# Kernel optimization log

Measured on AMD Instinct MI355X. Metric: run time of the kernel, lower is better.

The kernel has to match this reference:

```python
import jax, jax.numpy as jnp
import numpy as np

B, D, H, M, N, S = 256, 256, 512, 64, 2048, 3
SHIFTS = (1, 0, -1)  # = range(S//2, -S//2, -1); matches np.roll(eye, s, axis=1) one-hot matrices


def setup_inputs():
    key = jax.random.key(0)
    k = jax.random.split(key, 24)
    f32 = jnp.float32

    def rn(i, shape, scale):
        return jax.random.normal(k[i], shape, f32) * scale

    rh = jax.random.uniform(k[3], (B, N), f32)
    wh = jax.random.uniform(k[4], (B, N), f32)
    sc_ih = 1.0 / np.sqrt(D + M)
    sc_h = 1.0 / np.sqrt(H)
    return dict(
        inp=rn(0, (B, D), 1.0),
        h_tm1=rn(1, (B, H), 0.1),
        c_tm1=rn(2, (B, H), 0.1),
        read_head_tm1=rh / rh.sum(1, keepdims=True),
        write_head_tm1=wh / wh.sum(1, keepdims=True),
        memory=rn(5, (B, N, M), 0.5),
        W_ih=rn(6, (4 * H, D + M), sc_ih), W_hh=rn(7, (4 * H, H), sc_h),
        b_ih=jnp.zeros((4 * H,), f32), b_hh=jnp.zeros((4 * H,), f32),
        W_rk=rn(8, (M, H), sc_h), b_rk=rn(9, (M,), 0.01),
        W_wk=rn(10, (M, H), sc_h), b_wk=rn(11, (M,), 0.01),
        W_rc=rn(12, (3, H), sc_h), b_rc=jnp.zeros((3,), f32),
        W_wc=rn(13, (3, H), sc_h), b_wc=jnp.zeros((3,), f32),
        W_rs=rn(14, (S, H), sc_h), b_rs=jnp.zeros((S,), f32),
        W_ws=rn(15, (S, H), sc_h), b_ws=jnp.zeros((S,), f32),
        W_w=rn(16, (2 * M, H), sc_h), b_w=jnp.zeros((2 * M,), f32),
    )


def _head_params(h, Wk, bk, Wc, bc, Ws, bs):
    kk = jnp.tanh(h @ Wk.T + bk)                     # [B,M] key
    c = h @ Wc.T + bc                                # [B,3]
    beta = jax.nn.relu(c[:, 0:1]) + 1e-4             # focus strength
    g = jax.nn.sigmoid(c[:, 1:2])                    # interpolation gate
    gamma = jax.nn.relu(c[:, 2:3]) + 1.0001          # sharpening power
    s = jax.nn.softmax(h @ Ws.T + bs, axis=1)        # [B,S] shift weights
    return kk, s, beta, g, gamma


def _address(memory, head_tm1, kk, s, beta, g, gamma):
    dot = jnp.einsum('bm,bnm->bn', kk, memory)
    nk = jnp.linalg.norm(kk, axis=1, keepdims=True)  # [B,1]
    nM = jnp.linalg.norm(memory, axis=2)             # [B,N]
    cos = dot / jnp.maximum(nk * nM, 1e-8)
    content = jax.nn.softmax(beta * cos, axis=1)
    inter = g * content + (1.0 - g) * head_tm1       # gated interpolation [B,N]
    # circular shift; identical math to contracting with the one-hot C tensor
    rolled = jnp.stack([jnp.roll(inter, -sh, axis=1) for sh in SHIFTS], axis=1)  # [B,S,N]
    out = jnp.einsum('bsn,bs->bn', rolled, s)
    out = out ** gamma                               # sharpen
    return out / out.sum(1, keepdims=True)


def reference(inp, h_tm1, c_tm1, read_head_tm1, write_head_tm1, memory,
              W_ih, W_hh, b_ih, b_hh, W_rk, b_rk, W_wk, b_wk,
              W_rc, b_rc, W_wc, b_wc, W_rs, b_rs, W_ws, b_ws, W_w, b_w):
    # read addressing uses previous hidden state
    rp = _head_params(h_tm1, W_rk, b_rk, W_rc, b_rc, W_rs, b_rs)
    read_head = _address(memory, read_head_tm1, *rp)
    M_read = jnp.einsum('bn,bnm->bm', read_head, memory)  # [B,M]
    # LSTMCell controller (torch gate order i,f,g,o)
    x = jnp.concatenate([inp, M_read], axis=1)
    z = x @ W_ih.T + b_ih + h_tm1 @ W_hh.T + b_hh
    zi, zf, zg, zo = jnp.split(z, 4, axis=1)
    c_t = jax.nn.sigmoid(zf) * c_tm1 + jax.nn.sigmoid(zi) * jnp.tanh(zg)
    h_t = jax.nn.sigmoid(zo) * jnp.tanh(c_t)
    # write addressing uses new hidden state
    wp = _head_params(h_t, W_wk, b_wk, W_wc, b_wc, W_ws, b_ws)
    write_head = _address(memory, write_head_tm1, *wp)
    wa = h_t @ W_w.T + b_w
    e = jax.nn.sigmoid(wa[:, :M])                    # erase
    a = jnp.tanh(wa[:, M:])                          # add
    ww = write_head[:, :, None]                      # [B,N,1]
    M_out = memory * (1.0 - ww * e[:, None, :]) + ww * a[:, None, :]
    return (h_t, c_t, read_head, write_head, M_out)
```

## Files before the change

### kernel.cpp

```cpp
#include <hip/hip_runtime.h>
#include <hip/hip_bf16.h>

#define Bb 256
#define Dd 256
#define Hh 512
#define Mm 64
#define Nn 2048

typedef __attribute__((ext_vector_type(8))) short bf16x8;
typedef __attribute__((ext_vector_type(4))) float f32x4;

static __device__ __forceinline__ short f2bf(float f) {
    unsigned u = __float_as_uint(f);
    unsigned r = (u + 0x7FFFu + ((u >> 16) & 1u)) >> 16;
    return (short)r;
}

__global__ __launch_bounds__(256) void head_params_kernel(
    const float* __restrict__ h,
    const float* __restrict__ Wk, const float* __restrict__ bk,
    const float* __restrict__ Wc, const float* __restrict__ bc,
    const float* __restrict__ Ws, const float* __restrict__ bs,
    float* __restrict__ kk, float* __restrict__ par)
{
    int b = blockIdx.x;
    __shared__ float hs[Hh];
    __shared__ float red[6];
    __shared__ float skk[Mm];
    const float* hb = h + (size_t)b * Hh;
    for (int i = threadIdx.x; i < Hh; i += 256) hs[i] = hb[i];
    __syncthreads();

    int m   = threadIdx.x >> 2;
    int sub = threadIdx.x & 3;
    {
        const float* w = Wk + (size_t)m * Hh;
        float acc = 0.f;
        for (int k = sub * 128; k < sub * 128 + 128; ++k) acc += hs[k] * w[k];
        acc += __shfl_xor(acc, 1, 64);
        acc += __shfl_xor(acc, 2, 64);
        if (sub == 0) {
            float v = tanhf(acc + bk[m]);
            kk[(size_t)b * Mm + m] = v;
            skk[m] = v;
        }
    }
    if (threadIdx.x < 24) {
        int o  = threadIdx.x >> 2;
        int su = threadIdx.x & 3;
        const float* w = (o < 3) ? (Wc + (size_t)o * Hh) : (Ws + (size_t)(o - 3) * Hh);
        float acc = 0.f;
        for (int k = su * 128; k < su * 128 + 128; ++k) acc += hs[k] * w[k];
        acc += __shfl_xor(acc, 1, 64);
        acc += __shfl_xor(acc, 2, 64);
        if (su == 0) red[o] = acc + ((o < 3) ? bc[o] : bs[o - 3]);
    }
    __syncthreads();
    if (threadIdx.x == 0) {
        float c0 = red[0], c1 = red[1], c2 = red[2];
        float beta  = fmaxf(c0, 0.f) + 1e-4f;
        float g     = 1.f / (1.f + expf(-c1));
        float gamma = fmaxf(c2, 0.f) + 1.0001f;
        float l0 = red[3], l1 = red[4], l2 = red[5];
        float mx = fmaxf(l0, fmaxf(l1, l2));
        float e0 = expf(l0 - mx), e1 = expf(l1 - mx), e2 = expf(l2 - mx);
        float inv = 1.f / (e0 + e1 + e2);
        float ssq = 0.f;
        #pragma unroll
        for (int i = 0; i < Mm; ++i) ssq += skk[i] * skk[i];
        float* p = par + (size_t)b * 8;
        p[0] = beta; p[1] = g; p[2] = gamma;
        p[3] = e0 * inv; p[4] = e1 * inv; p[5] = e2 * inv;
        p[6] = sqrtf(ssq);
    }
}

template <int COMPUTE_NORM>
__global__ __launch_bounds__(256) void cos_pass_kernel(
    const float* __restrict__ mem, const float* __restrict__ kk,
    const float* __restrict__ par, float* __restrict__ cosv,
    float* __restrict__ nM)
{
    int b  = blockIdx.x >> 3;
    int n0 = (blockIdx.x & 7) << 8;
    int w  = threadIdx.x >> 6;
    int l  = threadIdx.x & 63;
    int m4 = l & 15;
    int rq = l >> 4;

    float4 kv = ((const float4*)(kk + (size_t)b * Mm))[m4];
    float kn = par[(size_t)b * 8 + 6];
    const float4* mb4 = (const float4*)(mem + (size_t)b * Nn * Mm);

    #pragma unroll
    for (int q = 0; q < 16; ++q) {
        int n = n0 + w * 64 + q * 4 + rq;
        size_t row = (size_t)b * Nn + n;
        float4 v = mb4[(size_t)n * 16 + m4];
        float dot = v.x * kv.x + v.y * kv.y + v.z * kv.z + v.w * kv.w;
        dot += __shfl_xor(dot, 1, 64);
        dot += __shfl_xor(dot, 2, 64);
        dot += __shfl_xor(dot, 4, 64);
        dot += __shfl_xor(dot, 8, 64);
        if (COMPUTE_NORM) {
            float ss = v.x * v.x + v.y * v.y + v.z * v.z + v.w * v.w;
            ss += __shfl_xor(ss, 1, 64);
            ss += __shfl_xor(ss, 2, 64);
            ss += __shfl_xor(ss, 4, 64);
            ss += __shfl_xor(ss, 8, 64);
            if (m4 == 0) {
                float nm = sqrtf(ss);
                nM[row] = nm;
                cosv[row] = dot / fmaxf(kn * nm, 1e-8f);
            }
        } else {
            if (m4 == 0) {
                float nm = nM[row];
                cosv[row] = dot / fmaxf(kn * nm, 1e-8f);
            }
        }
    }
}

__global__ __launch_bounds__(256) void address_kernel(
    const float* __restrict__ cosv, const float* __restrict__ par,
    const float* __restrict__ prev, float* __restrict__ outh)
{
    int b = blockIdx.x;
    __shared__ float sh[Nn];
    __shared__ float red[4];
    const float* cb = cosv + (size_t)b * Nn;
    const float* pv = par + (size_t)b * 8;
    float beta = pv[0], g = pv[1], gamma = pv[2];
    float s0 = pv[3], s1 = pv[4], s2 = pv[5];
    int tid = threadIdx.x;

    float vals[8];
    float mx = -1e30f;
    #pragma unroll
    for (int i = 0; i < 8; ++i) {
        float v = beta * cb[tid + i * 256];
        vals[i] = v;
        mx = fmaxf(mx, v);
    }
    #pragma unroll
    for (int msk = 1; msk < 64; msk <<= 1) mx = fmaxf(mx, __shfl_xor(mx, msk, 64));
    if ((tid & 63) == 0) red[tid >> 6] = mx;
    __syncthreads();
    mx = fmaxf(fmaxf(red[0], red[1]), fmaxf(red[2], red[3]));

    float sum = 0.f;
    #pragma unroll
    for (int i = 0; i < 8; ++i) {
        float e = expf(vals[i] - mx);
        vals[i] = e;
        sum += e;
    }
    #pragma unroll
    for (int msk = 1; msk < 64; msk <<= 1) sum += __shfl_xor(sum, msk, 64);
    __syncthreads();
    if ((tid & 63) == 0) red[tid >> 6] = sum;
    __syncthreads();
    sum = red[0] + red[1] + red[2] + red[3];
    float invs = 1.f / sum;

    const float* pb = prev + (size_t)b * Nn;
    #pragma unroll
    for (int i = 0; i < 8; ++i) {
        int n = tid + i * 256;
        sh[n] = g * vals[i] * invs + (1.f - g) * pb[n];
    }
    __syncthreads();

    float outs[8];
    float osum = 0.f;
    #pragma unroll
    for (int i = 0; i < 8; ++i) {
        int n = tid + i * 256;
        float v = s0 * sh[(n + 1) & (Nn - 1)] + s1 * sh[n] + s2 * sh[(n - 1) & (Nn - 1)];
        v = powf(v, gamma);
        outs[i] = v;
        osum += v;
    }
    #pragma unroll
    for (int msk = 1; msk < 64; msk <<= 1) osum += __shfl_xor(osum, msk, 64);
    __syncthreads();
    if ((tid & 63) == 0) red[tid >> 6] = osum;
    __syncthreads();
    osum = red[0] + red[1] + red[2] + red[3];
    float inv2 = 1.f / osum;
    #pragma unroll
    for (int i = 0; i < 8; ++i)
        outh[(size_t)b * Nn + tid + i * 256] = outs[i] * inv2;
}

__global__ __launch_bounds__(1024) void mread_kernel(
    const float* __restrict__ mem, const float* __restrict__ head,
    float* __restrict__ out)
{
    int b = blockIdx.x;
    int t = threadIdx.x;
    int m4 = t & 15;
    int r  = t >> 4;
    const float4* mb4 = (const float4*)(mem + (size_t)b * Nn * Mm);
    const float* hb = head + (size_t)b * Nn;
    float ax = 0.f, ay = 0.f, az = 0.f, aw = 0.f;
    for (int n = r; n < Nn; n += 64) {
        float wgt = hb[n];
        float4 v = mb4[(size_t)n * 16 + m4];
        ax += wgt * v.x; ay += wgt * v.y; az += wgt * v.z; aw += wgt * v.w;
    }
    __shared__ float4 red[64][16];
    red[r][m4] = make_float4(ax, ay, az, aw);
    __syncthreads();
    if (t < 256) {
        int g = t >> 4;
        float4 a = red[g * 4 + 0][m4], bq = red[g * 4 + 1][m4];
        float4 c = red[g * 4 + 2][m4], d  = red[g * 4 + 3][m4];
        red[g * 4][m4] = make_float4(a.x + bq.x + c.x + d.x, a.y + bq.y + c.y + d.y,
                                     a.z + bq.z + c.z + d.z, a.w + bq.w + c.w + d.w);
    }
    __syncthreads();
    if (t < 16) {
        float sx = 0.f, sy = 0.f, sz = 0.f, sw = 0.f;
        #pragma unroll
        for (int g = 0; g < 16; ++g) {
            float4 v = red[g * 4][t];
            sx += v.x; sy += v.y; sz += v.z; sw += v.w;
        }
        ((float4*)(out + (size_t)b * Mm))[t] = make_float4(sx, sy, sz, sw);
    }
}

__global__ __launch_bounds__(256) void convW_kernel(
    const float* __restrict__ W_ih, const float* __restrict__ W_hh,
    short* __restrict__ Wb)
{
    unsigned g = blockIdx.x * 256 + threadIdx.x;
    unsigned j = g / 104u;
    unsigned kq = (g - j * 104u) * 8u;
    const float* src = (kq < 320u) ? (W_ih + (size_t)j * 320 + kq)
                                   : (W_hh + (size_t)j * 512 + (kq - 320u));
    float4 a = ((const float4*)src)[0];
    float4 c = ((const float4*)src)[1];
    bf16x8 o;
    o[0] = f2bf(a.x); o[1] = f2bf(a.y); o[2] = f2bf(a.z); o[3] = f2bf(a.w);
    o[4] = f2bf(c.x); o[5] = f2bf(c.y); o[6] = f2bf(c.z); o[7] = f2bf(c.w);
    *(bf16x8*)(Wb + (size_t)j * 832 + kq) = o;
}

__global__ __launch_bounds__(256) void convA_kernel(
    const float* __restrict__ inp, const float* __restrict__ mrd,
    const float* __restrict__ h, short* __restrict__ Ab)
{
    unsigned g = blockIdx.x * 256 + threadIdx.x;
    unsigned r = g / 104u;
    unsigned kq = (g - r * 104u) * 8u;
    const float* src;
    if (kq < 256u)      src = inp + (size_t)r * 256 + kq;
    else if (kq < 320u) src = mrd + (size_t)r * 64 + (kq - 256u);
    else                src = h + (size_t)r * 512 + (kq - 320u);
    float4 a = ((const float4*)src)[0];
    float4 c = ((const float4*)src)[1];
    bf16x8 o;
    o[0] = f2bf(a.x); o[1] = f2bf(a.y); o[2] = f2bf(a.z); o[3] = f2bf(a.w);
    o[4] = f2bf(c.x); o[5] = f2bf(c.y); o[6] = f2bf(c.z); o[7] = f2bf(c.w);
    *(bf16x8*)(Ab + (size_t)r * 832 + kq) = o;
}

#define LDA 56
__global__ __launch_bounds__(256) void lstm_gemm_mfma(
    const short* __restrict__ Ab, const short* __restrict__ Wb,
    const float* __restrict__ b_ih, const float* __restrict__ b_hh,
    float* __restrict__ z)
{
    __shared__ short As[64][LDA];
    __shared__ short Bs[64][LDA];
    int t = threadIdx.x;
    int r0 = blockIdx.x * 64, c0 = blockIdx.y * 64;
    int w = t >> 6, l = t & 63;
    int wr = (w >> 1) * 32, wc = (w & 1) * 32;
    int ar = t >> 2, kq = (t & 3) * 8;
    int lr = l & 15, kb = (l >> 4) * 8;

    f32x4 acc00 = {0.f, 0.f, 0.f, 0.f}, acc01 = {0.f, 0.f, 0.f, 0.f};
    f32x4 acc10 = {0.f, 0.f, 0.f, 0.f}, acc11 = {0.f, 0.f, 0.f, 0.f};

    for (int kt = 0; kt < 26; ++kt) {
        int k0 = kt * 32;
        *(bf16x8*)&As[ar][kq] = *(const bf16x8*)(Ab + (size_t)(r0 + ar) * 832 + k0 + kq);
        *(bf16x8*)&Bs[ar][kq] = *(const bf16x8*)(Wb + (size_t)(c0 + ar) * 832 + k0 + kq);
        __syncthreads();
        bf16x8 a0 = *(const bf16x8*)&As[wr + lr][kb];
        bf16x8 a1 = *(const bf16x8*)&As[wr + 16 + lr][kb];
        bf16x8 b0 = *(const bf16x8*)&Bs[wc + lr][kb];
        bf16x8 b1 = *(const bf16x8*)&Bs[wc + 16 + lr][kb];
        acc00 = __builtin_amdgcn_mfma_f32_16x16x32_bf16(a0, b0, acc00, 0, 0, 0);
        acc01 = __builtin_amdgcn_mfma_f32_16x16x32_bf16(a0, b1, acc01, 0, 0, 0);
        acc10 = __builtin_amdgcn_mfma_f32_16x16x32_bf16(a1, b0, acc10, 0, 0, 0);
        acc11 = __builtin_amdgcn_mfma_f32_16x16x32_bf16(a1, b1, acc11, 0, 0, 0);
        __syncthreads();
    }
    int rq = (l >> 4) * 4;
    #pragma unroll
    for (int q = 0; q < 4; ++q) {
        int row0 = r0 + wr + rq + q;
        int col0 = c0 + wc + lr;
        z[(size_t)row0 * 2048 + col0] = acc00[q] + b_ih[col0] + b_hh[col0];
        z[(size_t)row0 * 2048 + col0 + 16] = acc01[q] + b_ih[col0 + 16] + b_hh[col0 + 16];
        z[(size_t)(row0 + 16) * 2048 + col0] = acc10[q] + b_ih[col0] + b_hh[col0];
        z[(size_t)(row0 + 16) * 2048 + col0 + 16] = acc11[q] + b_ih[col0 + 16] + b_hh[col0 + 16];
    }
}

__global__ __launch_bounds__(256) void gates_kernel(
    const float* __restrict__ z, const float* __restrict__ c_tm1,
    float* __restrict__ h_out, float* __restrict__ c_out)
{
    int idx = blockIdx.x * 256 + threadIdx.x;
    int b = idx >> 9, hh = idx & 511;
    const float* zb = z + (size_t)b * 2048;
    float zi = zb[hh], zf = zb[512 + hh], zg = zb[1024 + hh], zo = zb[1536 + hh];
    float si = 1.f / (1.f + expf(-zi));
    float sf = 1.f / (1.f + expf(-zf));
    float so = 1.f / (1.f + expf(-zo));
    float ct = sf * c_tm1[idx] + si * tanhf(zg);
    float ht = so * tanhf(ct);
    c_out[idx] = ct;
    h_out[idx] = ht;
}

__global__ __launch_bounds__(512) void wvec_kernel(
    const float* __restrict__ h, const float* __restrict__ W_w,
    const float* __restrict__ b_w, float* __restrict__ ea)
{
    int b = blockIdx.x;
    __shared__ float hs[Hh];
    for (int i = threadIdx.x; i < Hh; i += 512) hs[i] = h[(size_t)b * Hh + i];
    __syncthreads();
    int o  = threadIdx.x >> 2;
    int su = threadIdx.x & 3;
    const float* w = W_w + (size_t)o * Hh;
    float acc = 0.f;
    for (int k = su * 128; k < su * 128 + 128; ++k) acc += hs[k] * w[k];
    acc += __shfl_xor(acc, 1, 64);
    acc += __shfl_xor(acc, 2, 64);
    if (su == 0) {
        float v = acc + b_w[o];
        ea[(size_t)b * 128 + o] = (o < Mm) ? (1.f / (1.f + expf(-v))) : tanhf(v);
    }
}

__global__ __launch_bounds__(256) void mout_kernel(
    const float* __restrict__ mem, const float* __restrict__ head,
    const float* __restrict__ ea, float* __restrict__ out)
{
    size_t i4 = (size_t)blockIdx.x * 256 + threadIdx.x;
    size_t row = i4 >> 4;
    int m4 = (int)(i4 & 15);
    int b = (int)(row >> 11);
    float w = head[row];
    float4 mv = ((const float4*)mem)[i4];
    const float4* e4p = (const float4*)(ea + (size_t)b * 128);
    float4 ev = e4p[m4];
    float4 av = e4p[16 + m4];
    float4 o;
    o.x = mv.x * (1.f - w * ev.x) + w * av.x;
    o.y = mv.y * (1.f - w * ev.y) + w * av.y;
    o.z = mv.z * (1.f - w * ev.z) + w * av.z;
    o.w = mv.w * (1.f - w * ev.w) + w * av.w;
    ((float4*)out)[i4] = o;
}

extern "C" void kernel_launch(void* const* d_in, const int* in_sizes, int n_in,
                              void* d_out, int out_size, void* d_ws, size_t ws_size,
                              hipStream_t stream)
{
    const float* inp   = (const float*)d_in[0];
    const float* h_tm1 = (const float*)d_in[1];
    const float* c_tm1 = (const float*)d_in[2];
    const float* rh0   = (const float*)d_in[3];
    const float* wh0   = (const float*)d_in[4];
    const float* mem   = (const float*)d_in[5];
    const float* W_ih  = (const float*)d_in[6];
    const float* W_hh  = (const float*)d_in[7];
    const float* b_ih  = (const float*)d_in[8];
    const float* b_hh  = (const float*)d_in[9];
    const float* W_rk  = (const float*)d_in[10];
    const float* b_rk  = (const float*)d_in[11];
    const float* W_wk  = (const float*)d_in[12];
    const float* b_wk  = (const float*)d_in[13];
    const float* W_rc  = (const float*)d_in[14];
    const float* b_rc  = (const float*)d_in[15];
    const float* W_wc  = (const float*)d_in[16];
    const float* b_wc  = (const float*)d_in[17];
    const float* W_rs  = (const float*)d_in[18];
    const float* b_rs  = (const float*)d_in[19];
    const float* W_ws  = (const float*)d_in[20];
    const float* b_ws  = (const float*)d_in[21];
    const float* W_w   = (const float*)d_in[22];
    const float* b_w   = (const float*)d_in[23];

    float* out   = (float*)d_out;
    float* h_t   = out;
    float* c_t   = out + 131072;
    float* rhead = out + 262144;
    float* whead = out + 786432;
    float* mo    = out + 1310720;
    float* cosbuf = mo;
    float* zbuf   = mo + 524288;
    float* nMbuf  = mo + 1048576;
    short* Ab     = (short*)(mo + 1572864);
    short* Wb     = (short*)(mo + 1703936);

    float* ws  = (float*)d_ws;
    float* kk  = ws;
    float* par = ws + 16384;
    float* mrd = ws + 18432;
    float* ea  = ws + 34816;

    convW_kernel<<<832, 256, 0, stream>>>(W_ih, W_hh, Wb);

    head_params_kernel<<<Bb, 256, 0, stream>>>(h_tm1, W_rk, b_rk, W_rc, b_rc, W_rs, b_rs, kk, par);
    cos_pass_kernel<1><<<Bb * 8, 256, 0, stream>>>(mem, kk, par, cosbuf, nMbuf);
    address_kernel<<<Bb, 256, 0, stream>>>(cosbuf, par, rh0, rhead);
    mread_kernel<<<Bb, 1024, 0, stream>>>(mem, rhead, mrd);
    convA_kernel<<<104, 256, 0, stream>>>(inp, mrd, h_tm1, Ab);
    lstm_gemm_mfma<<<dim3(4, 32), 256, 0, stream>>>(Ab, Wb, b_ih, b_hh, zbuf);
    gates_kernel<<<Bb * Hh / 256, 256, 0, stream>>>(zbuf, c_tm1, h_t, c_t);

    head_params_kernel<<<Bb, 256, 0, stream>>>(h_t, W_wk, b_wk, W_wc, b_wc, W_ws, b_ws, kk, par);
    cos_pass_kernel<0><<<Bb * 8, 256, 0, stream>>>(mem, kk, par, cosbuf, nMbuf);
    address_kernel<<<Bb, 256, 0, stream>>>(cosbuf, par, wh0, whead);
    wvec_kernel<<<Bb, 512, 0, stream>>>(h_t, W_w, b_w, ea);
    mout_kernel<<<Bb * Nn * Mm / 4 / 256, 256, 0, stream>>>(mem, whead, ea, mo);
}
```

Measured before the change: 172.4 us.

## Fuse read addressing with memory read and write params with erase/add vectors

Merges the read-address softmax/shift/sharpen kernel with the weighted memory-read kernel, and the write head-param kernel with the erase/add vector kernel, so there are fewer launches and the read head stays in shared memory. It also swaps expf/powf for fast __expf and exp2/log2 intrinsics, unrolls the dot-product loops, and turns mout into a grid-stride loop over 2048 blocks. The Wb scratch offset moves as well. The fast-math intrinsics can cost a little accuracy, and the fused 1024-thread blocks may lower occupancy.

```diff
diff --git a/kernel.cpp b/kernel.cpp
--- a/kernel.cpp
+++ b/kernel.cpp
@@ -34,9 +34,11 @@
     int m   = threadIdx.x >> 2;
     int sub = threadIdx.x & 3;
     {
-        const float* w = Wk + (size_t)m * Hh;
+        const float* w = Wk + (size_t)m * Hh + sub * 128;
+        const float* hh = hs + sub * 128;
         float acc = 0.f;
-        for (int k = sub * 128; k < sub * 128 + 128; ++k) acc += hs[k] * w[k];
+        #pragma unroll 8
+        for (int k = 0; k < 128; ++k) acc += hh[k] * w[k];
         acc += __shfl_xor(acc, 1, 64);
         acc += __shfl_xor(acc, 2, 64);
         if (sub == 0) {
@@ -48,22 +50,23 @@
     if (threadIdx.x < 24) {
         int o  = threadIdx.x >> 2;
         int su = threadIdx.x & 3;
-        const float* w = (o < 3) ? (Wc + (size_t)o * Hh) : (Ws + (size_t)(o - 3) * Hh);
+        const float* w = ((o < 3) ? (Wc + (size_t)o * Hh) : (Ws + (size_t)(o - 3) * Hh)) + su * 128;
+        const float* hh = hs + su * 128;
         float acc = 0.f;
-        for (int k = su * 128; k < su * 128 + 128; ++k) acc += hs[k] * w[k];
+        #pragma unroll 8
+        for (int k = 0; k < 128; ++k) acc += hh[k] * w[k];
         acc += __shfl_xor(acc, 1, 64);
         acc += __shfl_xor(acc, 2, 64);
         if (su == 0) red[o] = acc + ((o < 3) ? bc[o] : bs[o - 3]);
     }
     __syncthreads();
     if (threadIdx.x == 0) {
-        float c0 = red[0], c1 = red[1], c2 = red[2];
-        float beta  = fmaxf(c0, 0.f) + 1e-4f;
-        float g     = 1.f / (1.f + expf(-c1));
-        float gamma = fmaxf(c2, 0.f) + 1.0001f;
+        float beta  = fmaxf(red[0], 0.f) + 1e-4f;
+        float g     = 1.f / (1.f + __expf(-red[1]));
+        float gamma = fmaxf(red[2], 0.f) + 1.0001f;
         float l0 = red[3], l1 = red[4], l2 = red[5];
         float mx = fmaxf(l0, fmaxf(l1, l2));
-        float e0 = expf(l0 - mx), e1 = expf(l1 - mx), e2 = expf(l2 - mx);
+        float e0 = __expf(l0 - mx), e1 = __expf(l1 - mx), e2 = __expf(l2 - mx);
         float inv = 1.f / (e0 + e1 + e2);
         float ssq = 0.f;
         #pragma unroll
@@ -72,6 +75,81 @@
         p[0] = beta; p[1] = g; p[2] = gamma;
         p[3] = e0 * inv; p[4] = e1 * inv; p[5] = e2 * inv;
         p[6] = sqrtf(ssq);
+    }
+}
+
+__global__ __launch_bounds__(1024) void wparams_wvec_kernel(
+    const float* __restrict__ h,
+    const float* __restrict__ Wk, const float* __restrict__ bk,
+    const float* __restrict__ Wc, const float* __restrict__ bc,
+    const float* __restrict__ Ws, const float* __restrict__ bs,
+    const float* __restrict__ W_w, const float* __restrict__ b_w,
+    float* __restrict__ kk, float* __restrict__ par, float* __restrict__ ea)
+{
+    int b = blockIdx.x;
+    int t = threadIdx.x;
+    __shared__ float hs[Hh];
+    __shared__ float red6[6];
+    __shared__ float skk[Mm];
+    if (t < Hh) hs[t] = h[(size_t)b * Hh + t];
+    __syncthreads();
+    if (t < 256) {
+        int m = t >> 2, sub = t & 3;
+        const float* w = Wk + (size_t)m * Hh + sub * 128;
+        const float* hh = hs + sub * 128;
+        float acc = 0.f;
+        #pragma unroll 8
+        for (int k = 0; k < 128; ++k) acc += hh[k] * w[k];
+        acc += __shfl_xor(acc, 1, 64);
+        acc += __shfl_xor(acc, 2, 64);
+        if (sub == 0) {
+            float v = tanhf(acc + bk[m]);
+            skk[m] = v;
+            kk[(size_t)b * Mm + m] = v;
+        }
+    } else if (t < 280) {
+        int o = (t - 256) >> 2, su = t & 3;
+        const float* w = ((o < 3) ? (Wc + (size_t)o * Hh) : (Ws + (size_t)(o - 3) * Hh)) + su * 128;
+        const float* hh = hs + su * 128;
+        float acc = 0.f;
+        #pragma unroll 8
+        for (int k = 0; k < 128; ++k) acc += hh[k] * w[k];
+        acc += __shfl_xor(acc, 1, 64);
+        acc += __shfl_xor(acc, 2, 64);
+        if (su == 0) red6[o] = acc + ((o < 3) ? bc[o] : bs[o - 3]);
+    } else if (t >= 512) {
+        int o = (t - 512) >> 2, su = t & 3;
+        const float* w = W_w + (size_t)o * Hh + su * 128;
+        const float* hh = hs + su * 128;
+        float acc = 0.f;
+        #pragma unroll 8
+        for (int k = 0; k < 128; ++k) acc += hh[k] * w[k];
+        acc += __shfl_xor(acc, 1, 64);
+        acc += __shfl_xor(acc, 2, 64);
+        if (su == 0) {
+            float v = acc + b_w[o];
+            ea[(size_t)b * 128 + o] = (o < Mm) ? (1.f / (1.f + __expf(-v))) : tanhf(v);
+        }
+    }
+    __syncthreads();
+    if (t < 64) {
+        float v = skk[t];
+        float ssq = v * v;
+        #pragma unroll
+        for (int msk = 1; msk < 64; msk <<= 1) ssq += __shfl_xor(ssq, msk, 64);
+        if (t == 0) {
+            float beta  = fmaxf(red6[0], 0.f) + 1e-4f;
+            float g     = 1.f / (1.f + __expf(-red6[1]));
+            float gamma = fmaxf(red6[2], 0.f) + 1.0001f;
+            float l0 = red6[3], l1 = red6[4], l2 = red6[5];
+            float mx = fmaxf(l0, fmaxf(l1, l2));
+            float e0 = __expf(l0 - mx), e1 = __expf(l1 - mx), e2 = __expf(l2 - mx);
+            float inv = 1.f / (e0 + e1 + e2);
+            float* p = par + (size_t)b * 8;
+            p[0] = beta; p[1] = g; p[2] = gamma;
+            p[3] = e0 * inv; p[4] = e1 * inv; p[5] = e2 * inv;
+            p[6] = sqrtf(ssq);
+        }
     }
 }
 
@@ -122,7 +200,101 @@
     }
 }
 
-__global__ __launch_bounds__(256) void address_kernel(
+__global__ __launch_bounds__(1024) void raddr_mread_kernel(
+    const float* __restrict__ cosv, const float* __restrict__ par,
+    const float* __restrict__ prev, const float* __restrict__ mem,
+    float* __restrict__ outh, float* __restrict__ mrd)
+{
+    int b = blockIdx.x;
+    int t = threadIdx.x;
+    int w = t >> 6, l = t & 63;
+    __shared__ float csh[Nn];
+    __shared__ float redw[16];
+    __shared__ float4 red4[64][16];
+
+    const float* pv = par + (size_t)b * 8;
+    float beta = pv[0], g = pv[1], gamma = pv[2];
+    float s0 = pv[3], s1 = pv[4], s2 = pv[5];
+
+    float v0 = beta * cosv[(size_t)b * Nn + t];
+    float v1 = beta * cosv[(size_t)b * Nn + t + 1024];
+    float mx = fmaxf(v0, v1);
+    #pragma unroll
+    for (int msk = 1; msk < 64; msk <<= 1) mx = fmaxf(mx, __shfl_xor(mx, msk, 64));
+    if (l == 0) redw[w] = mx;
+    __syncthreads();
+    mx = redw[0];
+    #pragma unroll
+    for (int i = 1; i < 16; ++i) mx = fmaxf(mx, redw[i]);
+    float e0 = __expf(v0 - mx), e1 = __expf(v1 - mx);
+    float sum = e0 + e1;
+    #pragma unroll
+    for (int msk = 1; msk < 64; msk <<= 1) sum += __shfl_xor(sum, msk, 64);
+    __syncthreads();
+    if (l == 0) redw[w] = sum;
+    __syncthreads();
+    sum = 0.f;
+    #pragma unroll
+    for (int i = 0; i < 16; ++i) sum += redw[i];
+    float invs = 1.f / sum;
+    const float* pb = prev + (size_t)b * Nn;
+    float i0 = g * e0 * invs + (1.f - g) * pb[t];
+    float i1 = g * e1 * invs + (1.f - g) * pb[t + 1024];
+    csh[t] = i0; csh[t + 1024] = i1;
+    __syncthreads();
+    int n1 = t + 1024;
+    float c0 = s0 * csh[(t + 1) & (Nn - 1)] + s1 * i0 + s2 * csh[(t - 1) & (Nn - 1)];
+    float c1 = s0 * csh[(n1 + 1) & (Nn - 1)] + s1 * i1 + s2 * csh[(n1 - 1) & (Nn - 1)];
+    float p0 = exp2f(gamma * __log2f(c0));
+    float p1 = exp2f(gamma * __log2f(c1));
+    float osum = p0 + p1;
+    #pragma unroll
+    for (int msk = 1; msk < 64; msk <<= 1) osum += __shfl_xor(osum, msk, 64);
+    __syncthreads();
+    if (l == 0) redw[w] = osum;
+    __syncthreads();
+    osum = 0.f;
+    #pragma unroll
+    for (int i = 0; i < 16; ++i) osum += redw[i];
+    float inv2 = 1.f / osum;
+    float h0 = p0 * inv2, h1 = p1 * inv2;
+    outh[(size_t)b * Nn + t] = h0;
+    outh[(size_t)b * Nn + n1] = h1;
+    __syncthreads();
+    csh[t] = h0; csh[n1] = h1;
+    __syncthreads();
+
+    int r = t >> 4;
+    int c = t & 15;
+    const float4* mb4 = (const float4*)(mem + (size_t)b * Nn * Mm);
+    float ax = 0.f, ay = 0.f, az = 0.f, aw = 0.f;
+    for (int n = r; n < Nn; n += 64) {
+        float wgt = csh[n];
+        float4 v = mb4[(size_t)n * 16 + c];
+        ax += wgt * v.x; ay += wgt * v.y; az += wgt * v.z; aw += wgt * v.w;
+    }
+    red4[r][c] = make_float4(ax, ay, az, aw);
+    __syncthreads();
+    if (t < 256) {
+        int gg = t >> 4, cc = t & 15;
+        float4 a = red4[gg * 4 + 0][cc], bq = red4[gg * 4 + 1][cc];
+        float4 cv = red4[gg * 4 + 2][cc], d = red4[gg * 4 + 3][cc];
+        red4[gg * 4][cc] = make_float4(a.x + bq.x + cv.x + d.x, a.y + bq.y + cv.y + d.y,
+                                       a.z + bq.z + cv.z + d.z, a.w + bq.w + cv.w + d.w);
+    }
+    __syncthreads();
+    if (t < 16) {
+        float sx = 0.f, sy = 0.f, sz = 0.f, sw = 0.f;
+        #pragma unroll
+        for (int gg = 0; gg < 16; ++gg) {
+            float4 v = red4[gg * 4][t];
+            sx += v.x; sy += v.y; sz += v.z; sw += v.w;
+        }
+        ((float4*)(mrd + (size_t)b * Mm))[t] = make_float4(sx, sy, sz, sw);
+    }
+}
+
+__global__ __launch_bounds__(256) void waddr_kernel(
     const float* __restrict__ cosv, const float* __restrict__ par,
     const float* __restrict__ prev, float* __restrict__ outh)
 {
@@ -152,7 +324,7 @@
     float sum = 0.f;
     #pragma unroll
     for (int i = 0; i < 8; ++i) {
-        float e = expf(vals[i] - mx);
+        float e = __expf(vals[i] - mx);
         vals[i] = e;
         sum += e;
     }
@@ -178,7 +350,7 @@
     for (int i = 0; i < 8; ++i) {
         int n = tid + i * 256;
         float v = s0 * sh[(n + 1) & (Nn - 1)] + s1 * sh[n] + s2 * sh[(n - 1) & (Nn - 1)];
-        v = powf(v, gamma);
+        v = exp2f(gamma * __log2f(v));
         outs[i] = v;
         osum += v;
     }
@@ -192,44 +364,6 @@
     #pragma unroll
     for (int i = 0; i < 8; ++i)
         outh[(size_t)b * Nn + tid + i * 256] = outs[i] * inv2;
-}
-
-__global__ __launch_bounds__(1024) void mread_kernel(
-    const float* __restrict__ mem, const float* __restrict__ head,
-    float* __restrict__ out)
-{
-    int b = blockIdx.x;
-    int t = threadIdx.x;
-    int m4 = t & 15;
-    int r  = t >> 4;
-    const float4* mb4 = (const float4*)(mem + (size_t)b * Nn * Mm);
-    const float* hb = head + (size_t)b * Nn;
-    float ax = 0.f, ay = 0.f, az = 0.f, aw = 0.f;
-    for (int n = r; n < Nn; n += 64) {
-        float wgt = hb[n];
-        float4 v = mb4[(size_t)n * 16 + m4];
-        ax += wgt * v.x; ay += wgt * v.y; az += wgt * v.z; aw += wgt * v.w;
-    }
-    __shared__ float4 red[64][16];
-    red[r][m4] = make_float4(ax, ay, az, aw);
-    __syncthreads();
-    if (t < 256) {
-        int g = t >> 4;
-        float4 a = red[g * 4 + 0][m4], bq = red[g * 4 + 1][m4];
-        float4 c = red[g * 4 + 2][m4], d  = red[g * 4 + 3][m4];
-        red[g * 4][m4] = make_float4(a.x + bq.x + c.x + d.x, a.y + bq.y + c.y + d.y,
-                                     a.z + bq.z + c.z + d.z, a.w + bq.w + c.w + d.w);
-    }
-    __syncthreads();
-    if (t < 16) {
-        float sx = 0.f, sy = 0.f, sz = 0.f, sw = 0.f;
-        #pragma unroll
-        for (int g = 0; g < 16; ++g) {
-            float4 v = red[g * 4][t];
-            sx += v.x; sy += v.y; sz += v.z; sw += v.w;
-        }
-        ((float4*)(out + (size_t)b * Mm))[t] = make_float4(sx, sy, sz, sw);
-    }
 }
 
 __global__ __launch_bounds__(256) void convW_kernel(
@@ -321,55 +455,37 @@
     int b = idx >> 9, hh = idx & 511;
     const float* zb = z + (size_t)b * 2048;
     float zi = zb[hh], zf = zb[512 + hh], zg = zb[1024 + hh], zo = zb[1536 + hh];
-    float si = 1.f / (1.f + expf(-zi));
-    float sf = 1.f / (1.f + expf(-zf));
-    float so = 1.f / (1.f + expf(-zo));
+    float si = 1.f / (1.f + __expf(-zi));
+    float sf = 1.f / (1.f + __expf(-zf));
+    float so = 1.f / (1.f + __expf(-zo));
     float ct = sf * c_tm1[idx] + si * tanhf(zg);
     float ht = so * tanhf(ct);
     c_out[idx] = ct;
     h_out[idx] = ht;
 }
 
-__global__ __launch_bounds__(512) void wvec_kernel(
-    const float* __restrict__ h, const float* __restrict__ W_w,
-    const float* __restrict__ b_w, float* __restrict__ ea)
-{
-    int b = blockIdx.x;
-    __shared__ float hs[Hh];
-    for (int i = threadIdx.x; i < Hh; i += 512) hs[i] = h[(size_t)b * Hh + i];
-    __syncthreads();
-    int o  = threadIdx.x >> 2;
-    int su = threadIdx.x & 3;
-    const float* w = W_w + (size_t)o * Hh;
-    float acc = 0.f;
-    for (int k = su * 128; k < su * 128 + 128; ++k) acc += hs[k] * w[k];
-    acc += __shfl_xor(acc, 1, 64);
-    acc += __shfl_xor(acc, 2, 64);
-    if (su == 0) {
-        float v = acc + b_w[o];
-        ea[(size_t)b * 128 + o] = (o < Mm) ? (1.f / (1.f + expf(-v))) : tanhf(v);
-    }
-}
-
 __global__ __launch_bounds__(256) void mout_kernel(
     const float* __restrict__ mem, const float* __restrict__ head,
     const float* __restrict__ ea, float* __restrict__ out)
 {
-    size_t i4 = (size_t)blockIdx.x * 256 + threadIdx.x;
-    size_t row = i4 >> 4;
-    int m4 = (int)(i4 & 15);
-    int b = (int)(row >> 11);
-    float w = head[row];
-    float4 mv = ((const float4*)mem)[i4];
-    const float4* e4p = (const float4*)(ea + (size_t)b * 128);
-    float4 ev = e4p[m4];
-    float4 av = e4p[16 + m4];
-    float4 o;
-    o.x = mv.x * (1.f - w * ev.x) + w * av.x;
-    o.y = mv.y * (1.f - w * ev.y) + w * av.y;
-    o.z = mv.z * (1.f - w * ev.z) + w * av.z;
-    o.w = mv.w * (1.f - w * ev.w) + w * av.w;
-    ((float4*)out)[i4] = o;
+    const size_t total = (size_t)Bb * Nn * Mm / 4;
+    for (size_t i4 = (size_t)blockIdx.x * 256 + threadIdx.x; i4 < total;
+         i4 += (size_t)2048 * 256) {
+        size_t row = i4 >> 4;
+        int m4 = (int)(i4 & 15);
+        int b = (int)(row >> 11);
+        float w = head[row];
+        float4 mv = ((const float4*)mem)[i4];
+        const float4* e4p = (const float4*)(ea + (size_t)b * 128);
+        float4 ev = e4p[m4];
+        float4 av = e4p[16 + m4];
+        float4 o;
+        o.x = mv.x * (1.f - w * ev.x) + w * av.x;
+        o.y = mv.y * (1.f - w * ev.y) + w * av.y;
+        o.z = mv.z * (1.f - w * ev.z) + w * av.z;
+        o.w = mv.w * (1.f - w * ev.w) + w * av.w;
+        ((float4*)out)[i4] = o;
+    }
 }
 
 extern "C" void kernel_launch(void* const* d_in, const int* in_sizes, int n_in,
@@ -411,7 +527,7 @@
     float* zbuf   = mo + 524288;
     float* nMbuf  = mo + 1048576;
     short* Ab     = (short*)(mo + 1572864);
-    short* Wb     = (short*)(mo + 1703936);
+    short* Wb     = (short*)(mo + 1679360);
 
     float* ws  = (float*)d_ws;
     float* kk  = ws;
@@ -423,15 +539,14 @@
 
     head_params_kernel<<<Bb, 256, 0, stream>>>(h_tm1, W_rk, b_rk, W_rc, b_rc, W_rs, b_rs, kk, par);
     cos_pass_kernel<1><<<Bb * 8, 256, 0, stream>>>(mem, kk, par, cosbuf, nMbuf);
-    address_kernel<<<Bb, 256, 0, stream>>>(cosbuf, par, rh0, rhead);
-    mread_kernel<<<Bb, 1024, 0, stream>>>(mem, rhead, mrd);
+    raddr_mread_kernel<<<Bb, 1024, 0, stream>>>(cosbuf, par, rh0, mem, rhead, mrd);
     convA_kernel<<<104, 256, 0, stream>>>(inp, mrd, h_tm1, Ab);
     lstm_gemm_mfma<<<dim3(4, 32), 256, 0, stream>>>(Ab, Wb, b_ih, b_hh, zbuf);
     gates_kernel<<<Bb * Hh / 256, 256, 0, stream>>>(zbuf, c_tm1, h_t, c_t);
 
-    head_params_kernel<<<Bb, 256, 0, stream>>>(h_t, W_wk, b_wk, W_wc, b_wc, W_ws, b_ws, kk, par);
+    wparams_wvec_kernel<<<Bb, 1024, 0, stream>>>(
+        h_t, W_wk, b_wk, W_wc, b_wc, W_ws, b_ws, W_w, b_w, kk, par, ea);
     cos_pass_kernel<0><<<Bb * 8, 256, 0, stream>>>(mem, kk, par, cosbuf, nMbuf);
-    address_kernel<<<Bb, 256, 0, stream>>>(cosbuf, par, wh0, whead);
-    wvec_kernel<<<Bb, 512, 0, stream>>>(h_t, W_w, b_w, ea);
-    mout_kernel<<<Bb * Nn * Mm / 4 / 256, 256, 0, stream>>>(mem, whead, ea, mo);
-}
+    waddr_kernel<<<Bb, 256, 0, stream>>>(cosbuf, par, wh0, whead);
+    mout_kernel<<<2048, 256, 0, stream>>>(mem, whead, ea, mo);
+}
```

Result: faster. 166.9 us (-3.2%).
